# Performance work log

Measured on AMD Instinct MI355X. Metric: run time of the kernel, lower is better.

Reference implementation:

```python
import jax, jax.numpy as jnp
import numpy as np

B, S, D = 4, 2048, 512
H, DK = 8, 64
LN_EPS = 1e-5


def setup_inputs() -> dict:
    key = jax.random.key(0)
    ks = jax.random.split(key, 10)
    scale = 1.0 / np.sqrt(D)
    inp = {
        "input_Q": jax.random.normal(ks[0], (B, S, D), jnp.float32),
        "input_K": jax.random.normal(ks[1], (B, S, D), jnp.float32),
        "input_V": jax.random.normal(ks[2], (B, S, D), jnp.float32),
        # causal mask: True = masked (upper triangle), broadcast to batch
        "attn_mask": jnp.broadcast_to(
            jnp.triu(jnp.ones((S, S), jnp.bool_), k=1), (B, S, S)
        ),
        # Linear(d_model, d_k*n_heads, bias=False) weights, stored as [in, out]
        "W_Q": jax.random.normal(ks[3], (D, H * DK), jnp.float32) * scale,
        "W_K": jax.random.normal(ks[4], (D, H * DK), jnp.float32) * scale,
        "W_V": jax.random.normal(ks[5], (D, H * DK), jnp.float32) * scale,
        "W_fc": jax.random.normal(ks[6], (H * DK, D), jnp.float32) * scale,
        "ln_gamma": jnp.ones((D,), jnp.float32),
        "ln_beta": jnp.zeros((D,), jnp.float32),
    }
    return inp


def reference(input_Q, input_K, input_V, attn_mask, W_Q, W_K, W_V, W_fc, ln_gamma, ln_beta):
    # projections -> [B, H, S, DK]
    q = (input_Q @ W_Q).reshape(B, S, H, DK).transpose(0, 2, 1, 3)
    k = (input_K @ W_K).reshape(B, S, H, DK).transpose(0, 2, 1, 3)
    v = (input_V @ W_V).reshape(B, S, H, DK).transpose(0, 2, 1, 3)

    # scores: [B, H, S, S]
    scores = jnp.einsum("bhqd,bhkd->bhqk", q, k) / jnp.sqrt(jnp.float32(DK))
    scores = jnp.where(attn_mask[:, None, :, :], jnp.float32(-1e9), scores)
    attn = jax.nn.softmax(scores, axis=-1)

    # context: [B, S, H*DK]
    context = jnp.einsum("bhqk,bhkd->bhqd", attn, v)
    context = context.transpose(0, 2, 1, 3).reshape(B, S, H * DK)

    output = context @ W_fc + input_Q  # residual

    # LayerNorm over last dim
    mu = jnp.mean(output, axis=-1, keepdims=True)
    var = jnp.var(output, axis=-1, keepdims=True)
    return (output - mu) / jnp.sqrt(var + LN_EPS) * ln_gamma + ln_beta
```

## Files before the change

### kernel.cpp

```cpp
#include <hip/hip_runtime.h>
#include <hip/hip_bf16.h>
#include <stdint.h>

#define DEV __device__ __forceinline__

using f32x4  = __attribute__((ext_vector_type(4))) float;
using bf16x8 = __attribute__((ext_vector_type(8))) short;
using u16x4  = __attribute__((ext_vector_type(4))) unsigned short;
using u16x8  = __attribute__((ext_vector_type(8))) unsigned short;
using u32x4  = __attribute__((ext_vector_type(4))) uint32_t;

DEV uint16_t f2b(float f) {
  uint32_t u = __builtin_bit_cast(uint32_t, f);
  uint32_t r = u + 0x7FFFu + ((u >> 16) & 1u);
  return (uint16_t)(r >> 16);
}
DEV float b2f(uint16_t h) {
  return __builtin_bit_cast(float, (uint32_t)h << 16);
}

DEV uint32_t cvtpk(float lo, float hi) {
  uint32_t r;
  asm("v_cvt_pk_bf16_f32 %0, %1, %2" : "=v"(r) : "v"(lo), "v"(hi));
  return r;
}

DEV void gload16(const void* g, void* l) {
  __builtin_amdgcn_global_load_lds((__attribute__((address_space(1))) void*)g,
                                   (__attribute__((address_space(3))) void*)l,
                                   16, 0, 0);
}

DEV bf16x8 ldsfrag(const uint16_t* base, int row, int cb) {
  int b = row * 128 + (cb ^ ((row & 7) << 4));
  return *(const bf16x8*)((const uint8_t*)base + b);
}

DEV f32x4 MFMA(bf16x8 a, bf16x8 b, f32x4 c) {
  return __builtin_amdgcn_mfma_f32_16x16x32_bf16(a, b, c, 0, 0, 0);
}

__global__ void k_convert3(const float* __restrict__ A0, const float* __restrict__ A1,
                           const float* __restrict__ A2, uint16_t* __restrict__ O0,
                           uint16_t* __restrict__ O1, uint16_t* __restrict__ O2) {
  const int z = blockIdx.z;
  const float* in = (z == 0) ? A0 : (z == 1) ? A1 : A2;
  uint16_t* out = (z == 0) ? O0 : (z == 1) ? O1 : O2;
  int i = blockIdx.x * blockDim.x + threadIdx.x;
  int stride = gridDim.x * blockDim.x;
  for (; i < 1048576; i += stride) {
    f32x4 v = ((const f32x4*)in)[i];
    u16x4 o;
    o[0] = f2b(v[0]); o[1] = f2b(v[1]); o[2] = f2b(v[2]); o[3] = f2b(v[3]);
    ((u16x4*)out)[i] = o;
  }
}

__global__ void k_wtrans4(const float* __restrict__ W0, const float* __restrict__ W1,
                          const float* __restrict__ W2, const float* __restrict__ W3,
                          uint16_t* __restrict__ WtBase, float scale0) {
  __shared__ float t[32][33];
  const int z = blockIdx.z;
  const float* W = (z == 0) ? W0 : (z == 1) ? W1 : (z == 2) ? W2 : W3;
  const float scale = (z == 0) ? scale0 : 1.0f;
  uint16_t* Wt = WtBase + (size_t)z * 262144;
  int tx = threadIdx.x, ty = threadIdx.y;
  int n0 = blockIdx.x * 32, k0 = blockIdx.y * 32;
#pragma unroll
  for (int i = 0; i < 4; ++i)
    t[ty + 8 * i][tx] = W[(size_t)(k0 + ty + 8 * i) * 512 + n0 + tx];
  __syncthreads();
#pragma unroll
  for (int i = 0; i < 4; ++i)
    Wt[(size_t)(n0 + ty + 8 * i) * 512 + k0 + tx] = f2b(t[tx][ty + 8 * i] * scale);
}

DEV void stage_gemm(const uint8_t* Ab, const uint8_t* Bb, int m0, int n0, int kt,
                    uint16_t* As, uint16_t* Bs, int wid, int l8, int cb0) {
#pragma unroll
  for (int i = 0; i < 4; ++i) {
    int inst = wid + i * 4;
    int row = inst * 8 + l8;
    int cbs = cb0 ^ ((row & 7) << 4);
    gload16(Ab + (size_t)(m0 + row) * 1024 + kt * 128 + cbs, (uint8_t*)As + inst * 1024);
  }
#pragma unroll
  for (int i = 0; i < 2; ++i) {
    int inst = wid + i * 4;
    int row = inst * 8 + l8;
    int cbs = cb0 ^ ((row & 7) << 4);
    gload16(Bb + (size_t)(n0 + row) * 1024 + kt * 128 + cbs, (uint8_t*)Bs + inst * 1024);
  }
}

__global__ __launch_bounds__(256) void k_gemm_qkv(const uint16_t* __restrict__ A0,
                                                  const uint16_t* __restrict__ A1,
                                                  const uint16_t* __restrict__ A2,
                                                  const uint16_t* __restrict__ WtBase,
                                                  uint16_t* __restrict__ O0,
                                                  uint16_t* __restrict__ O1,
                                                  uint16_t* __restrict__ O2, int zbase) {
  __shared__ uint16_t As[2][8192];
  __shared__ uint16_t Bs[2][4096];
  const int z = blockIdx.z + zbase;
  const uint16_t* A = (z == 0) ? A0 : (z == 1) ? A1 : A2;
  uint16_t* out = (z == 0) ? O0 : (z == 1) ? O1 : O2;
  const uint8_t* Ab = (const uint8_t*)A;
  const uint8_t* Bb = (const uint8_t*)(WtBase + (size_t)z * 262144);
  const int tid = threadIdx.x, lane = tid & 63, wid = tid >> 6;
  const int g = lane >> 4, c16 = lane & 15;
  const int wm = wid & 1, wn = wid >> 1;
  const int m0 = blockIdx.x * 128, n0 = blockIdx.y * 64;
  const int l8 = lane >> 3, cb0 = (lane & 7) << 4;

  f32x4 acc[4][2] = {};

  stage_gemm(Ab, Bb, m0, n0, 0, As[0], Bs[0], wid, l8, cb0);
  __syncthreads();

  for (int kt = 0; kt < 8; ++kt) {
    const int cur = kt & 1;
    if (kt < 7)
      stage_gemm(Ab, Bb, m0, n0, kt + 1, As[cur ^ 1], Bs[cur ^ 1], wid, l8, cb0);
    const uint16_t* Ac = As[cur];
    const uint16_t* Bc = Bs[cur];
#pragma unroll
    for (int ks = 0; ks < 2; ++ks) {
      int cb = ks * 64 + (g << 4);
      bf16x8 af[4], bfr[2];
#pragma unroll
      for (int mi = 0; mi < 4; ++mi) af[mi] = ldsfrag(Ac, wm * 64 + mi * 16 + c16, cb);
#pragma unroll
      for (int ni = 0; ni < 2; ++ni) bfr[ni] = ldsfrag(Bc, wn * 32 + ni * 16 + c16, cb);
#pragma unroll
      for (int mi = 0; mi < 4; ++mi)
#pragma unroll
        for (int ni = 0; ni < 2; ++ni)
          acc[mi][ni] = MFMA(af[mi], bfr[ni], acc[mi][ni]);
    }
    __syncthreads();
  }

  const int lm = g * 4;
  if (z != 2) {
#pragma unroll
    for (int mi = 0; mi < 4; ++mi)
#pragma unroll
      for (int ni = 0; ni < 2; ++ni)
#pragma unroll
        for (int r = 0; r < 4; ++r) {
          int m = m0 + wm * 64 + mi * 16 + lm + r;
          int n = n0 + wn * 32 + ni * 16 + c16;
          size_t a = (size_t)((m >> 11) * 8 + (n >> 6)) * 131072 + (size_t)(m & 2047) * 64 + (n & 63);
          out[a] = f2b(acc[mi][ni][r]);
        }
  } else {
#pragma unroll
    for (int mi = 0; mi < 4; ++mi)
#pragma unroll
      for (int ni = 0; ni < 2; ++ni) {
        int m = m0 + wm * 64 + mi * 16 + lm;
        int n = n0 + wn * 32 + ni * 16 + c16;
        u16x4 w;
#pragma unroll
        for (int r = 0; r < 4; ++r) w[r] = f2b(acc[mi][ni][r]);
        size_t a = (size_t)((m >> 11) * 8 + (n >> 6)) * 131072 + (size_t)(n & 63) * 2048 + (m & 2047);
        *(u16x4*)(out + a) = w;
      }
  }
}

__global__ __launch_bounds__(256) void k_gemm_fc(const uint16_t* __restrict__ A,
                                                 const uint16_t* __restrict__ Bt,
                                                 uint16_t* __restrict__ out) {
  __shared__ uint16_t As[2][8192];
  __shared__ uint16_t Bs[2][4096];
  const int tid = threadIdx.x, lane = tid & 63, wid = tid >> 6;
  const int g = lane >> 4, c16 = lane & 15;
  const int wm = wid & 1, wn = wid >> 1;
  const int m0 = blockIdx.x * 128, n0 = blockIdx.y * 64;
  const uint8_t* Ab = (const uint8_t*)A;
  const uint8_t* Bb = (const uint8_t*)Bt;
  const int l8 = lane >> 3, cb0 = (lane & 7) << 4;

  f32x4 acc[4][2] = {};

  stage_gemm(Ab, Bb, m0, n0, 0, As[0], Bs[0], wid, l8, cb0);
  __syncthreads();

  for (int kt = 0; kt < 8; ++kt) {
    const int cur = kt & 1;
    if (kt < 7)
      stage_gemm(Ab, Bb, m0, n0, kt + 1, As[cur ^ 1], Bs[cur ^ 1], wid, l8, cb0);
    const uint16_t* Ac = As[cur];
    const uint16_t* Bc = Bs[cur];
#pragma unroll
    for (int ks = 0; ks < 2; ++ks) {
      int cb = ks * 64 + (g << 4);
      bf16x8 af[4], bfr[2];
#pragma unroll
      for (int mi = 0; mi < 4; ++mi) af[mi] = ldsfrag(Ac, wm * 64 + mi * 16 + c16, cb);
#pragma unroll
      for (int ni = 0; ni < 2; ++ni) bfr[ni] = ldsfrag(Bc, wn * 32 + ni * 16 + c16, cb);
#pragma unroll
      for (int mi = 0; mi < 4; ++mi)
#pragma unroll
        for (int ni = 0; ni < 2; ++ni)
          acc[mi][ni] = MFMA(af[mi], bfr[ni], acc[mi][ni]);
    }
    __syncthreads();
  }

  const int lm = g * 4;
#pragma unroll
  for (int mi = 0; mi < 4; ++mi)
#pragma unroll
    for (int ni = 0; ni < 2; ++ni)
#pragma unroll
      for (int r = 0; r < 4; ++r) {
        int m = m0 + wm * 64 + mi * 16 + lm + r;
        int n = n0 + wn * 32 + ni * 16 + c16;
        out[(size_t)m * 512 + n] = f2b(acc[mi][ni][r]);
      }
}

DEV void stageK(const uint8_t* kb, int kt, uint16_t* Ks, int wid, int l8, int cb0) {
#pragma unroll
  for (int i = 0; i < 2; ++i) {
    int inst = wid + i * 4;
    int rho = inst * 8 + l8;
    int f = rho >> 4, g2 = (rho >> 2) & 3, r = rho & 3;
    int s_loc = ((f & 1) << 5) | (g2 << 3) | ((f >> 1) << 2) | r;
    int cbs = cb0 ^ ((rho & 7) << 4);
    gload16(kb + (size_t)(kt * 64 + s_loc) * 128 + cbs, (uint8_t*)Ks + inst * 1024);
  }
}
DEV void stageV(const uint8_t* vb, int kt, uint16_t* Vs, int wid, int l8, int cb0) {
#pragma unroll
  for (int i = 0; i < 2; ++i) {
    int inst = wid + i * 4;
    int row = inst * 8 + l8;
    int cbs = cb0 ^ ((row & 7) << 4);
    gload16(vb + (size_t)row * 4096 + (size_t)kt * 128 + cbs, (uint8_t*)Vs + inst * 1024);
  }
}

__global__ __launch_bounds__(256) void k_attn(const uint16_t* __restrict__ qg,
                                              const uint16_t* __restrict__ kg,
                                              const uint16_t* __restrict__ vtg,
                                              uint16_t* __restrict__ ctxg) {
  const int x = blockIdx.x, bh = blockIdx.y;
  const int gx = (x & 1) ? (x >> 1) : 31 - (x >> 1);
  const int qi = ((bh >> 3) & 1) ? 31 - gx : gx;

  const int tid = threadIdx.x, lane = tid & 63, wid = tid >> 6;
  const int g = lane >> 4, qcol = lane & 15;
  __shared__ uint16_t smem[4 * 4096];
  const uint8_t* qb = (const uint8_t*)(qg + (size_t)bh * 131072);
  const uint8_t* kb = (const uint8_t*)(kg + (size_t)bh * 131072);
  const uint8_t* vb = (const uint8_t*)(vtg + (size_t)bh * 131072);
  const int l8 = lane >> 3, cb0 = (lane & 7) << 4;
  const int qrow_w = qi * 64 + wid * 16;

  bf16x8 qf[2];
  {
    const uint8_t* qrow = qb + (size_t)(qrow_w + qcol) * 128;
    qf[0] = *(const bf16x8*)(qrow + (g << 4));
    qf[1] = *(const bf16x8*)(qrow + 64 + (g << 4));
  }

  stageK(kb, 0, smem, wid, l8, cb0);
  stageV(vb, 0, smem + 8192, wid, l8, cb0);
  __syncthreads();

  bf16x8 ones;
#pragma unroll
  for (int j = 0; j < 8; ++j) ones[j] = (short)0x3F80;

  f32x4 oacc[4] = {};
  f32x4 lacc = {};
  const int nkt = qi + 1;

  for (int kt = 0; kt < nkt; ++kt) {
    const int cur = kt & 1;
    if (kt + 1 < nkt) {
      stageK(kb, kt + 1, smem + ((cur ^ 1) << 12), wid, l8, cb0);
      stageV(vb, kt + 1, smem + 8192 + ((cur ^ 1) << 12), wid, l8, cb0);
    }
    const uint16_t* Kc = smem + (cur << 12);
    const uint16_t* Vc = smem + 8192 + (cur << 12);

    f32x4 sacc[4] = {};
#pragma unroll
    for (int ks2 = 0; ks2 < 2; ++ks2) {
      int cb = ks2 * 64 + (g << 4);
#pragma unroll
      for (int sf = 0; sf < 4; ++sf) {
        bf16x8 kf = ldsfrag(Kc, sf * 16 + qcol, cb);
        sacc[sf] = MFMA(kf, qf[ks2], sacc[sf]);
      }
    }

    if (kt * 64 + 63 > qrow_w) {
      int q_glob = qrow_w + qcol;
#pragma unroll
      for (int sf = 0; sf < 4; ++sf)
#pragma unroll
        for (int r = 0; r < 4; ++r) {
          int s_glob = kt * 64 + (((sf & 1) << 5) | (g << 3) | ((sf >> 1) << 2) | r);
          if (s_glob > q_glob) sacc[sf][r] = -1e30f;
        }
    }

    float p[4][4];
#pragma unroll
    for (int sf = 0; sf < 4; ++sf)
#pragma unroll
      for (int r = 0; r < 4; ++r) p[sf][r] = __builtin_amdgcn_exp2f(sacc[sf][r]);

#pragma unroll
    for (int ks = 0; ks < 2; ++ks) {
      u32x4 tv;
      tv[0] = cvtpk(p[ks][0], p[ks][1]);
      tv[1] = cvtpk(p[ks][2], p[ks][3]);
      tv[2] = cvtpk(p[2 + ks][0], p[2 + ks][1]);
      tv[3] = cvtpk(p[2 + ks][2], p[2 + ks][3]);
      bf16x8 pb = __builtin_bit_cast(bf16x8, tv);
      lacc = MFMA(ones, pb, lacc);
#pragma unroll
      for (int dkf = 0; dkf < 4; ++dkf) {
        bf16x8 vf = ldsfrag(Vc, dkf * 16 + qcol, ks * 64 + (g << 4));
        oacc[dkf] = MFMA(vf, pb, oacc[dkf]);
      }
    }
    __syncthreads();
  }

  uint16_t* Os = smem + wid * 1024;
  {
    float iv = 1.f / lacc[0];
    int q_l = qcol;
#pragma unroll
    for (int dkf = 0; dkf < 4; ++dkf) {
      u16x4 w;
#pragma unroll
      for (int r = 0; r < 4; ++r) w[r] = f2b(oacc[dkf][r] * iv);
      int dkb = dkf * 32 + g * 8;
      int bo = q_l * 128 + (dkb ^ ((q_l & 7) << 4));
      *(u16x4*)((uint8_t*)Os + bo) = w;
    }
  }
  __syncthreads();
  const int bb = bh >> 3, hh = bh & 7;
#pragma unroll
  for (int j = 0; j < 2; ++j) {
    int lin = j * 1024 + lane * 16;
    int q_l = lin >> 7;
    int cb = lin & 127;
    int bo = q_l * 128 + (cb ^ ((q_l & 7) << 4));
    bf16x8 val = *(const bf16x8*)((const uint8_t*)(smem + wid * 1024) + bo);
    size_t ga = (size_t)(bb * 2048 + qrow_w + q_l) * 512 + hh * 64 + (cb >> 1);
    *(bf16x8*)(ctxg + ga) = val;
  }
}

__global__ __launch_bounds__(256) void k_ln(const uint16_t* __restrict__ fc,
                                            const float* __restrict__ resid,
                                            const float* __restrict__ gamma,
                                            const float* __restrict__ beta,
                                            float* __restrict__ out) {
  int row = blockIdx.x * 4 + (threadIdx.x >> 6);
  int lane = threadIdx.x & 63;
  const uint16_t* fr = fc + (size_t)row * 512 + lane * 8;
  const float* rr = resid + (size_t)row * 512 + lane * 8;
  u16x8 fv = *(const u16x8*)fr;
  f32x4 c = *(const f32x4*)rr;
  f32x4 d = *(const f32x4*)(rr + 4);
  float y[8];
#pragma unroll
  for (int j = 0; j < 4; ++j) { y[j] = b2f(fv[j]) + c[j]; y[4 + j] = b2f(fv[4 + j]) + d[j]; }
  float s = 0.f, s2 = 0.f;
#pragma unroll
  for (int j = 0; j < 8; ++j) { s += y[j]; s2 = fmaf(y[j], y[j], s2); }
#pragma unroll
  for (int off = 1; off < 64; off <<= 1) {
    s += __shfl_xor(s, off);
    s2 += __shfl_xor(s2, off);
  }
  float mean = s * (1.f / 512.f);
  float var = s2 * (1.f / 512.f) - mean * mean;
  float rstd = rsqrtf(var + 1e-5f);
  f32x4 o0, o1;
#pragma unroll
  for (int j = 0; j < 4; ++j) {
    o0[j] = (y[j] - mean) * rstd * gamma[lane * 8 + j] + beta[lane * 8 + j];
    o1[j] = (y[4 + j] - mean) * rstd * gamma[lane * 8 + 4 + j] + beta[lane * 8 + 4 + j];
  }
  float* op = out + (size_t)row * 512 + lane * 8;
  *(f32x4*)op = o0;
  *(f32x4*)(op + 4) = o1;
}

extern "C" void kernel_launch(void* const* d_in, const int* in_sizes, int n_in,
                              void* d_out, int out_size, void* d_ws, size_t ws_size,
                              hipStream_t stream) {
  const float* inQ = (const float*)d_in[0];
  const float* inK = (const float*)d_in[1];
  const float* inV = (const float*)d_in[2];
  const float* Wq = (const float*)d_in[4];
  const float* Wk = (const float*)d_in[5];
  const float* Wv = (const float*)d_in[6];
  const float* Wfc = (const float*)d_in[7];
  const float* gamma = (const float*)d_in[8];
  const float* beta = (const float*)d_in[9];
  uint8_t* ws = (uint8_t*)d_ws;
  const size_t MB = 1048576;

  uint16_t* Wt  = (uint16_t*)(ws + 0);
  uint16_t* Xb0 = (uint16_t*)(ws + 2 * MB);
  uint16_t* Xb1 = (uint16_t*)(ws + 10 * MB);
  uint16_t* Xb2 = (uint16_t*)(ws + 18 * MB);
  const bool fused = ws_size >= 52 * MB;

  uint16_t *Qb, *Kb, *Vtb, *Ctx, *Fc;
  if (fused) {
    Qb  = (uint16_t*)(ws + 26 * MB);
    Kb  = (uint16_t*)(ws + 34 * MB);
    Vtb = (uint16_t*)(ws + 42 * MB);
    Ctx = (uint16_t*)(ws + 2 * MB);
    Fc  = (uint16_t*)(ws + 10 * MB);
  } else {
    Qb  = (uint16_t*)(ws + 26 * MB);
    Kb  = (uint16_t*)(ws + 34 * MB);
    Vtb = (uint16_t*)(ws + 2 * MB);
    Ctx = (uint16_t*)(ws + 10 * MB);
    Fc  = (uint16_t*)(ws + 18 * MB);
  }
  float* out = (float*)d_out;

  dim3 b256(256);
  dim3 tb(32, 8), tg4(16, 16, 4);
  k_wtrans4<<<tg4, tb, 0, stream>>>(Wq, Wk, Wv, Wfc, Wt, 0.18033688011112042f);

  dim3 cg(1024, 1, 3);
  k_convert3<<<cg, b256, 0, stream>>>(inQ, inK, inV, Xb0, Xb1, Xb2);

  if (fused) {
    dim3 gq(64, 8, 3);
    k_gemm_qkv<<<gq, b256, 0, stream>>>(Xb0, Xb1, Xb2, Wt, Qb, Kb, Vtb, 0);
  } else {
    dim3 gq(64, 8, 1);
    k_gemm_qkv<<<gq, b256, 0, stream>>>(Xb0, Xb1, Xb2, Wt, Qb, Kb, Vtb, 0);
    k_gemm_qkv<<<gq, b256, 0, stream>>>(Xb0, Xb1, Xb2, Wt, Qb, Kb, Vtb, 1);
    k_gemm_qkv<<<gq, b256, 0, stream>>>(Xb0, Xb1, Xb2, Wt, Qb, Kb, Vtb, 2);
  }

  dim3 ag(32, 32);
  k_attn<<<ag, b256, 0, stream>>>(Qb, Kb, Vtb, Ctx);

  dim3 gg(64, 8);
  k_gemm_fc<<<gg, b256, 0, stream>>>(Ctx, Wt + 3 * 262144, Fc);
  k_ln<<<2048, b256, 0, stream>>>(Fc, inQ, gamma, beta, out);
}
```

Measured before the change: 90.61 us.

## Load K and V fragments directly from global memory, drop LDS staging

The attention kernel no longer stages K and V tiles into double-buffered shared memory. Each wave now reads its MFMA fragments straight from global memory, which removes the per-iteration block barriers and shrinks shared memory to a small per-wave output buffer. In exchange, the four waves of a block each fetch the same K/V data redundantly through the cache, and load latency is no longer hidden by the async prefetch of the next tile. The block barrier before the output readback is also removed, which looks safe only because each wave reads back just its own region.

```diff
diff --git a/kernel.cpp b/kernel.cpp
--- a/kernel.cpp
+++ b/kernel.cpp
@@ -224,27 +224,6 @@
       }
 }
 
-DEV void stageK(const uint8_t* kb, int kt, uint16_t* Ks, int wid, int l8, int cb0) {
-#pragma unroll
-  for (int i = 0; i < 2; ++i) {
-    int inst = wid + i * 4;
-    int rho = inst * 8 + l8;
-    int f = rho >> 4, g2 = (rho >> 2) & 3, r = rho & 3;
-    int s_loc = ((f & 1) << 5) | (g2 << 3) | ((f >> 1) << 2) | r;
-    int cbs = cb0 ^ ((rho & 7) << 4);
-    gload16(kb + (size_t)(kt * 64 + s_loc) * 128 + cbs, (uint8_t*)Ks + inst * 1024);
-  }
-}
-DEV void stageV(const uint8_t* vb, int kt, uint16_t* Vs, int wid, int l8, int cb0) {
-#pragma unroll
-  for (int i = 0; i < 2; ++i) {
-    int inst = wid + i * 4;
-    int row = inst * 8 + l8;
-    int cbs = cb0 ^ ((row & 7) << 4);
-    gload16(vb + (size_t)row * 4096 + (size_t)kt * 128 + cbs, (uint8_t*)Vs + inst * 1024);
-  }
-}
-
 __global__ __launch_bounds__(256) void k_attn(const uint16_t* __restrict__ qg,
                                               const uint16_t* __restrict__ kg,
                                               const uint16_t* __restrict__ vtg,
@@ -255,11 +234,10 @@
 
   const int tid = threadIdx.x, lane = tid & 63, wid = tid >> 6;
   const int g = lane >> 4, qcol = lane & 15;
-  __shared__ uint16_t smem[4 * 4096];
+  __shared__ uint16_t smem[4][1024];
   const uint8_t* qb = (const uint8_t*)(qg + (size_t)bh * 131072);
   const uint8_t* kb = (const uint8_t*)(kg + (size_t)bh * 131072);
   const uint8_t* vb = (const uint8_t*)(vtg + (size_t)bh * 131072);
-  const int l8 = lane >> 3, cb0 = (lane & 7) << 4;
   const int qrow_w = qi * 64 + wid * 16;
 
   bf16x8 qf[2];
@@ -269,9 +247,10 @@
     qf[1] = *(const bf16x8*)(qrow + 64 + (g << 4));
   }
 
-  stageK(kb, 0, smem, wid, l8, cb0);
-  stageV(vb, 0, smem + 8192, wid, l8, cb0);
-  __syncthreads();
+  int srow[4];
+#pragma unroll
+  for (int sf = 0; sf < 4; ++sf)
+    srow[sf] = ((sf & 1) << 5) | ((qcol >> 2) << 3) | ((sf >> 1) << 2) | (qcol & 3);
 
   bf16x8 ones;
 #pragma unroll
@@ -282,21 +261,13 @@
   const int nkt = qi + 1;
 
   for (int kt = 0; kt < nkt; ++kt) {
-    const int cur = kt & 1;
-    if (kt + 1 < nkt) {
-      stageK(kb, kt + 1, smem + ((cur ^ 1) << 12), wid, l8, cb0);
-      stageV(vb, kt + 1, smem + 8192 + ((cur ^ 1) << 12), wid, l8, cb0);
-    }
-    const uint16_t* Kc = smem + (cur << 12);
-    const uint16_t* Vc = smem + 8192 + (cur << 12);
-
     f32x4 sacc[4] = {};
 #pragma unroll
     for (int ks2 = 0; ks2 < 2; ++ks2) {
-      int cb = ks2 * 64 + (g << 4);
 #pragma unroll
       for (int sf = 0; sf < 4; ++sf) {
-        bf16x8 kf = ldsfrag(Kc, sf * 16 + qcol, cb);
+        bf16x8 kf = *(const bf16x8*)(kb + (size_t)(kt * 64 + srow[sf]) * 128 +
+                                     ks2 * 64 + (g << 4));
         sacc[sf] = MFMA(kf, qf[ks2], sacc[sf]);
       }
     }
@@ -329,14 +300,14 @@
       lacc = MFMA(ones, pb, lacc);
 #pragma unroll
       for (int dkf = 0; dkf < 4; ++dkf) {
-        bf16x8 vf = ldsfrag(Vc, dkf * 16 + qcol, ks * 64 + (g << 4));
+        bf16x8 vf = *(const bf16x8*)(vb + (size_t)(dkf * 16 + qcol) * 4096 +
+                                     kt * 128 + ks * 64 + (g << 4));
         oacc[dkf] = MFMA(vf, pb, oacc[dkf]);
       }
     }
-    __syncthreads();
-  }
-
-  uint16_t* Os = smem + wid * 1024;
+  }
+
+  uint16_t* Os = smem[wid];
   {
     float iv = 1.f / lacc[0];
     int q_l = qcol;
@@ -350,7 +321,6 @@
       *(u16x4*)((uint8_t*)Os + bo) = w;
     }
   }
-  __syncthreads();
   const int bb = bh >> 3, hh = bh & 7;
 #pragma unroll
   for (int j = 0; j < 2; ++j) {
@@ -358,7 +328,7 @@
     int q_l = lin >> 7;
     int cb = lin & 127;
     int bo = q_l * 128 + (cb ^ ((q_l & 7) << 4));
-    bf16x8 val = *(const bf16x8*)((const uint8_t*)(smem + wid * 1024) + bo);
+    bf16x8 val = *(const bf16x8*)((const uint8_t*)Os + bo);
     size_t ga = (size_t)(bb * 2048 + qrow_w + q_l) * 512 + hh * 64 + (cb >> 1);
     *(bf16x8*)(ctxg + ga) = val;
   }
```

New measurement: 189.7 us. 2.09x slower.

## Fuse fp32-to-bf16 input conversion into QKV projection GEMM

Applied to the files above, without the earlier changes.

Drops the separate conversion kernel and has the QKV GEMM stream fp32 inputs directly into LDS through async global-to-LDS loads, using a new XOR-swizzled 256-byte-row layout. The fp32 fragments are converted to bf16 in registers with v_cvt_pk_bf16_f32 just before the MFMAs. This removes one kernel launch and the write and re-read of a 24 MB bf16 intermediate. In exchange the GEMM now reads fp32 (twice the A-operand traffic per tile), uses double the LDS for the A buffers, adds conversion ALU work in the inner loop, and reorganizes the workspace layout, dropping the non-fused fallback.

```diff
diff --git a/kernel.cpp b/kernel.cpp
--- a/kernel.cpp
+++ b/kernel.cpp
@@ -38,22 +38,6 @@
 
 DEV f32x4 MFMA(bf16x8 a, bf16x8 b, f32x4 c) {
   return __builtin_amdgcn_mfma_f32_16x16x32_bf16(a, b, c, 0, 0, 0);
-}
-
-__global__ void k_convert3(const float* __restrict__ A0, const float* __restrict__ A1,
-                           const float* __restrict__ A2, uint16_t* __restrict__ O0,
-                           uint16_t* __restrict__ O1, uint16_t* __restrict__ O2) {
-  const int z = blockIdx.z;
-  const float* in = (z == 0) ? A0 : (z == 1) ? A1 : A2;
-  uint16_t* out = (z == 0) ? O0 : (z == 1) ? O1 : O2;
-  int i = blockIdx.x * blockDim.x + threadIdx.x;
-  int stride = gridDim.x * blockDim.x;
-  for (; i < 1048576; i += stride) {
-    f32x4 v = ((const f32x4*)in)[i];
-    u16x4 o;
-    o[0] = f2b(v[0]); o[1] = f2b(v[1]); o[2] = f2b(v[2]); o[3] = f2b(v[3]);
-    ((u16x4*)out)[i] = o;
-  }
 }
 
 __global__ void k_wtrans4(const float* __restrict__ W0, const float* __restrict__ W1,
@@ -93,17 +77,37 @@
   }
 }
 
-__global__ __launch_bounds__(256) void k_gemm_qkv(const uint16_t* __restrict__ A0,
-                                                  const uint16_t* __restrict__ A1,
-                                                  const uint16_t* __restrict__ A2,
+DEV void stageB(const uint8_t* Bb, int n0, int kt, uint16_t* Bs, int wid, int l8, int cb0) {
+#pragma unroll
+  for (int i = 0; i < 2; ++i) {
+    int inst = wid + i * 4;
+    int row = inst * 8 + l8;
+    int cbs = cb0 ^ ((row & 7) << 4);
+    gload16(Bb + (size_t)(n0 + row) * 1024 + kt * 128 + cbs, (uint8_t*)Bs + inst * 1024);
+  }
+}
+
+DEV void stageA32(const uint8_t* Ab, int m0, int kt, uint8_t* Albuf, int wid, int lane) {
+#pragma unroll
+  for (int i = 0; i < 8; ++i) {
+    int inst = wid + i * 4;
+    int row = inst * 4 + (lane >> 4);
+    int csrc = (lane & 15) ^ (row & 15);
+    gload16(Ab + (size_t)(m0 + row) * 2048 + kt * 256 + csrc * 16, Albuf + inst * 1024);
+  }
+}
+
+__global__ __launch_bounds__(256) void k_gemm_qkv(const float* __restrict__ inQ,
+                                                  const float* __restrict__ inK,
+                                                  const float* __restrict__ inV,
                                                   const uint16_t* __restrict__ WtBase,
                                                   uint16_t* __restrict__ O0,
                                                   uint16_t* __restrict__ O1,
-                                                  uint16_t* __restrict__ O2, int zbase) {
-  __shared__ uint16_t As[2][8192];
+                                                  uint16_t* __restrict__ O2) {
+  __shared__ float Af[2][8192];
   __shared__ uint16_t Bs[2][4096];
-  const int z = blockIdx.z + zbase;
-  const uint16_t* A = (z == 0) ? A0 : (z == 1) ? A1 : A2;
+  const int z = blockIdx.z;
+  const float* A = (z == 0) ? inQ : (z == 1) ? inK : inV;
   uint16_t* out = (z == 0) ? O0 : (z == 1) ? O1 : O2;
   const uint8_t* Ab = (const uint8_t*)A;
   const uint8_t* Bb = (const uint8_t*)(WtBase + (size_t)z * 262144);
@@ -115,21 +119,37 @@
 
   f32x4 acc[4][2] = {};
 
-  stage_gemm(Ab, Bb, m0, n0, 0, As[0], Bs[0], wid, l8, cb0);
+  stageA32(Ab, m0, 0, (uint8_t*)Af[0], wid, lane);
+  stageB(Bb, n0, 0, Bs[0], wid, l8, cb0);
   __syncthreads();
 
   for (int kt = 0; kt < 8; ++kt) {
     const int cur = kt & 1;
-    if (kt < 7)
-      stage_gemm(Ab, Bb, m0, n0, kt + 1, As[cur ^ 1], Bs[cur ^ 1], wid, l8, cb0);
-    const uint16_t* Ac = As[cur];
+    if (kt < 7) {
+      stageA32(Ab, m0, kt + 1, (uint8_t*)Af[cur ^ 1], wid, lane);
+      stageB(Bb, n0, kt + 1, Bs[cur ^ 1], wid, l8, cb0);
+    }
+    const uint8_t* Ac = (const uint8_t*)Af[cur];
     const uint16_t* Bc = Bs[cur];
 #pragma unroll
     for (int ks = 0; ks < 2; ++ks) {
+      bf16x8 af[4], bfr[2];
+#pragma unroll
+      for (int mi = 0; mi < 4; ++mi) {
+        int row = wm * 64 + mi * 16 + c16;
+        int r15 = row & 15;
+        const uint8_t* rb = Ac + row * 256;
+        int c0 = ks * 8 + g * 2;
+        f32x4 lo = *(const f32x4*)(rb + ((c0 ^ r15) << 4));
+        f32x4 hi = *(const f32x4*)(rb + (((c0 + 1) ^ r15) << 4));
+        u32x4 w;
+        w[0] = cvtpk(lo[0], lo[1]);
+        w[1] = cvtpk(lo[2], lo[3]);
+        w[2] = cvtpk(hi[0], hi[1]);
+        w[3] = cvtpk(hi[2], hi[3]);
+        af[mi] = __builtin_bit_cast(bf16x8, w);
+      }
       int cb = ks * 64 + (g << 4);
-      bf16x8 af[4], bfr[2];
-#pragma unroll
-      for (int mi = 0; mi < 4; ++mi) af[mi] = ldsfrag(Ac, wm * 64 + mi * 16 + c16, cb);
 #pragma unroll
       for (int ni = 0; ni < 2; ++ni) bfr[ni] = ldsfrag(Bc, wn * 32 + ni * 16 + c16, cb);
 #pragma unroll
@@ -417,43 +437,19 @@
   const size_t MB = 1048576;
 
   uint16_t* Wt  = (uint16_t*)(ws + 0);
-  uint16_t* Xb0 = (uint16_t*)(ws + 2 * MB);
-  uint16_t* Xb1 = (uint16_t*)(ws + 10 * MB);
-  uint16_t* Xb2 = (uint16_t*)(ws + 18 * MB);
-  const bool fused = ws_size >= 52 * MB;
-
-  uint16_t *Qb, *Kb, *Vtb, *Ctx, *Fc;
-  if (fused) {
-    Qb  = (uint16_t*)(ws + 26 * MB);
-    Kb  = (uint16_t*)(ws + 34 * MB);
-    Vtb = (uint16_t*)(ws + 42 * MB);
-    Ctx = (uint16_t*)(ws + 2 * MB);
-    Fc  = (uint16_t*)(ws + 10 * MB);
-  } else {
-    Qb  = (uint16_t*)(ws + 26 * MB);
-    Kb  = (uint16_t*)(ws + 34 * MB);
-    Vtb = (uint16_t*)(ws + 2 * MB);
-    Ctx = (uint16_t*)(ws + 10 * MB);
-    Fc  = (uint16_t*)(ws + 18 * MB);
-  }
+  uint16_t* Qb  = (uint16_t*)(ws + 2 * MB);
+  uint16_t* Kb  = (uint16_t*)(ws + 10 * MB);
+  uint16_t* Vtb = (uint16_t*)(ws + 18 * MB);
+  uint16_t* Ctx = (uint16_t*)(ws + 26 * MB);
+  uint16_t* Fc  = (uint16_t*)(ws + 34 * MB);
   float* out = (float*)d_out;
 
   dim3 b256(256);
   dim3 tb(32, 8), tg4(16, 16, 4);
   k_wtrans4<<<tg4, tb, 0, stream>>>(Wq, Wk, Wv, Wfc, Wt, 0.18033688011112042f);
 
-  dim3 cg(1024, 1, 3);
-  k_convert3<<<cg, b256, 0, stream>>>(inQ, inK, inV, Xb0, Xb1, Xb2);
-
-  if (fused) {
-    dim3 gq(64, 8, 3);
-    k_gemm_qkv<<<gq, b256, 0, stream>>>(Xb0, Xb1, Xb2, Wt, Qb, Kb, Vtb, 0);
-  } else {
-    dim3 gq(64, 8, 1);
-    k_gemm_qkv<<<gq, b256, 0, stream>>>(Xb0, Xb1, Xb2, Wt, Qb, Kb, Vtb, 0);
-    k_gemm_qkv<<<gq, b256, 0, stream>>>(Xb0, Xb1, Xb2, Wt, Qb, Kb, Vtb, 1);
-    k_gemm_qkv<<<gq, b256, 0, stream>>>(Xb0, Xb1, Xb2, Wt, Qb, Kb, Vtb, 2);
-  }
+  dim3 gq(64, 8, 3);
+  k_gemm_qkv<<<gq, b256, 0, stream>>>(inQ, inK, inV, Wt, Qb, Kb, Vtb);
 
   dim3 ag(32, 32);
   k_attn<<<ag, b256, 0, stream>>>(Qb, Kb, Vtb, Ctx);
```

New measurement: 91.48 us. Within noise of the previous version (+1.0%).
